# Performance work log

Measured on AMD Instinct MI355X. Metric: run time of the kernel, lower is better.

## Reference

```python
import jax, jax.numpy as jnp
import numpy as np

B, L, H, P = 128, 40, 256, 256   # n_mols, max_num_atoms, pc_hidden, pred_hidden
NS, NC, NB = 40, 5, 5            # n_SYMBOLS, n_FORMAL_CHARGES, n_BOND_TYPES


def _lin(key, fan_in, fan_out):
    kw, kb = jax.random.split(key)
    s = 1.0 / np.sqrt(fan_in)
    W = jax.random.uniform(kw, (fan_out, fan_in), minval=-s, maxval=s, dtype=jnp.float32)
    b = jax.random.uniform(kb, (fan_out,), minval=-s, maxval=s, dtype=jnp.float32)
    return W, b


def setup_inputs() -> dict:
    key = jax.random.key(0)
    ks = jax.random.split(key, 7)
    x = jax.random.normal(ks[0], (B, L, H), dtype=jnp.float32)
    W1s, b1s = _lin(ks[1], H, P)
    W2s, b2s = _lin(ks[2], P, NS)
    W1c, b1c = _lin(ks[3], H, P)
    W2c, b2c = _lin(ks[4], P, NC)
    W1b, b1b = _lin(ks[5], 2 * H, 2 * P)
    W2b, b2b = _lin(ks[6], 2 * P, NB)
    return dict(x_embedding=x, W1s=W1s, b1s=b1s, W2s=W2s, b2s=b2s,
                W1c=W1c, b1c=b1c, W2c=W2c, b2c=b2c,
                W1b=W1b, b1b=b1b, W2b=W2b, b2b=b2b)


def reference(x_embedding, W1s, b1s, W2s, b2s, W1c, b1c, W2c, b2c, W1b, b1b, W2b, b2b):
    lrelu = lambda v: jax.nn.leaky_relu(v, 0.01)
    y = x_embedding  # [B, L, H]; every molecule has ley == L (max_num_atoms)

    # symbol / charge heads: small FFNs applied per atom
    symbols = lrelu(jnp.einsum('blh,ph->blp', y, W1s) + b1s) @ W2s.T + b2s
    symbols = symbols.reshape(-1, NS)                       # [B*L, NS]
    charges = lrelu(jnp.einsum('blh,ph->blp', y, W1c) + b1c) @ W2c.T + b2c
    charges = charges.reshape(-1, NC)                       # [B*L, NC]

    # pairwise bond features: concat(atom_i, atom_j) -> [B, L, L, 2H]
    x1 = jnp.broadcast_to(y[:, :, None, :], (B, L, L, H))
    x2 = jnp.broadcast_to(y[:, None, :, :], (B, L, L, H))
    pair = jnp.concatenate([x1, x2], axis=-1)
    hb = lrelu(jnp.einsum('bijc,pc->bijp', pair, W1b) + b1b)  # [B, L, L, 2P]
    bl = jnp.einsum('bijp,np->bijn', hb, W2b) + b2b           # [B, L, L, NB]
    bl = bl + jnp.swapaxes(bl, 1, 2)                          # symmetrize

    # diagonal override: bond types 0..3 -> -1000, type 4 ('no bond') -> +1000
    eye = jnp.eye(L, dtype=bool)[None, :, :, None]
    diagvals = jnp.array([-1000.0, -1000.0, -1000.0, -1000.0, 1000.0], dtype=bl.dtype)
    bl = jnp.where(eye, diagvals, bl)
    bonds = bl.reshape(-1, NB)                                # [B*L*L, NB]

    return (symbols, charges, bonds)
```

## Files before the change

kernel.cpp:

```cpp
#include <hip/hip_runtime.h>
#include <hip/hip_fp16.h>

#define NMOL 128
#define LMAX 40
#define HDIM 256
#define NSYM 40
#define NCHG 5
#define NROWS (NMOL * LMAX)

typedef __attribute__((ext_vector_type(8))) unsigned short ushx8;
typedef __attribute__((ext_vector_type(8))) _Float16 f16x8;
typedef __attribute__((ext_vector_type(2))) _Float16 f16x2;
typedef __attribute__((ext_vector_type(2))) __fp16 fp16x2r;
typedef __attribute__((ext_vector_type(4))) float f32x4;

__device__ __forceinline__ float lrelu(float x) { return fmaxf(x, 0.01f * x); }

__global__ __launch_bounds__(256) void gemm_kernel(
    const float* __restrict__ x,
    const float* __restrict__ W1s, const float* __restrict__ b1s,
    const float* __restrict__ W1c, const float* __restrict__ b1c,
    const float* __restrict__ W1b, const float* __restrict__ b1b,
    _Float16* __restrict__ hout, _Float16* __restrict__ uvp)
{
    __shared__ _Float16 As[64 * 256];
    __shared__ _Float16 Bs[64 * 256];

    const int t  = threadIdx.x;
    const int m0 = blockIdx.x * 64;
    const int n0 = blockIdx.y * 64;

    const float* Bsrc; int bstride; const float* bias_src;
    if (n0 < 256)       { Bsrc = W1s + (size_t)n0 * 256;            bstride = 256; bias_src = b1s + n0; }
    else if (n0 < 512)  { Bsrc = W1c + (size_t)(n0 - 256) * 256;    bstride = 256; bias_src = b1c + (n0 - 256); }
    else if (n0 < 1024) { Bsrc = W1b + (size_t)(n0 - 512) * 512;    bstride = 512; bias_src = b1b + (n0 - 512); }
    else                { Bsrc = W1b + (size_t)(n0 - 1024) * 512 + 256; bstride = 512; bias_src = nullptr; }

    #pragma unroll
    for (int pass = 0; pass < 8; ++pass) {
        int gch = pass * 256 + t;
        int r = gch >> 5, c = gch & 31;
        int cs = c ^ (r & 7);
        {
            const float* s = x + (size_t)(m0 + r) * 256 + c * 8;
            float4 a0 = *(const float4*)s, a1 = *(const float4*)(s + 4);
            union { f16x8 v; fp16x2r p[4]; } u;
            u.p[0] = __builtin_amdgcn_cvt_pkrtz(a0.x, a0.y);
            u.p[1] = __builtin_amdgcn_cvt_pkrtz(a0.z, a0.w);
            u.p[2] = __builtin_amdgcn_cvt_pkrtz(a1.x, a1.y);
            u.p[3] = __builtin_amdgcn_cvt_pkrtz(a1.z, a1.w);
            *(f16x8*)&As[r * 256 + cs * 8] = u.v;
        }
        {
            const float* s = Bsrc + (size_t)r * bstride + c * 8;
            float4 a0 = *(const float4*)s, a1 = *(const float4*)(s + 4);
            union { f16x8 v; fp16x2r p[4]; } u;
            u.p[0] = __builtin_amdgcn_cvt_pkrtz(a0.x, a0.y);
            u.p[1] = __builtin_amdgcn_cvt_pkrtz(a0.z, a0.w);
            u.p[2] = __builtin_amdgcn_cvt_pkrtz(a1.x, a1.y);
            u.p[3] = __builtin_amdgcn_cvt_pkrtz(a1.z, a1.w);
            *(f16x8*)&Bs[r * 256 + cs * 8] = u.v;
        }
    }
    __syncthreads();

    const int lane = t & 63, wave = t >> 6;
    const int wm = (wave >> 1) * 32, wn = (wave & 1) * 32;
    const int lr = lane & 15, lk = lane >> 4;

    f32x4 acc[2][2] = {};
    #pragma unroll
    for (int ks = 0; ks < 8; ++ks) {
        f16x8 a[2], b[2];
        #pragma unroll
        for (int i = 0; i < 2; ++i) {
            int ra = wm + i * 16 + lr;
            int ca = (ks * 4 + lk) ^ (ra & 7);
            a[i] = *(const f16x8*)&As[ra * 256 + ca * 8];
            int rb = wn + i * 16 + lr;
            int cb = (ks * 4 + lk) ^ (rb & 7);
            b[i] = *(const f16x8*)&Bs[rb * 256 + cb * 8];
        }
        #pragma unroll
        for (int mi = 0; mi < 2; ++mi)
            #pragma unroll
            for (int ni = 0; ni < 2; ++ni)
                acc[mi][ni] = __builtin_amdgcn_mfma_f32_16x16x32_f16(a[mi], b[ni], acc[mi][ni], 0, 0, 0);
    }

    #pragma unroll
    for (int mi = 0; mi < 2; ++mi) {
        #pragma unroll
        for (int ni = 0; ni < 2; ++ni) {
            int nl = wn + ni * 16 + lr;
            int ng = n0 + nl;
            float bs = bias_src ? bias_src[nl] : 0.0f;
            #pragma unroll
            for (int rg = 0; rg < 4; ++rg) {
                int row = m0 + wm + mi * 16 + lk * 4 + rg;
                float v = acc[mi][ni][rg] + bs;
                if (ng < 512) hout[(size_t)row * 512 + ng] = (_Float16)lrelu(v);
                else          uvp[(size_t)row * 1024 + (ng - 512)] = (_Float16)v;
            }
        }
    }
}

__global__ __launch_bounds__(256) void heads2_kernel(
    const _Float16* __restrict__ h,
    const float* __restrict__ W2s, const float* __restrict__ b2s,
    const float* __restrict__ W2c, const float* __restrict__ b2c,
    float* __restrict__ out_sym, float* __restrict__ out_chg)
{
    __shared__ unsigned short hsd[8 * 512];
    const int t = threadIdx.x;
    const int r0 = blockIdx.x * 8;
    #pragma unroll
    for (int pass = 0; pass < 2; ++pass) {
        int ch = pass * 256 + t;
        *(ushx8*)&hsd[ch * 8] = *(const ushx8*)((const unsigned short*)h + (size_t)r0 * 512 + ch * 8);
    }
    __syncthreads();

    for (int idx = t; idx < 8 * (NSYM + NCHG); idx += 256) {
        int r = idx / (NSYM + NCHG), m = idx % (NSYM + NCHG);
        bool is_sym = (m < NSYM);
        int n = is_sym ? m : m - NSYM;
        const unsigned short* hrow = &hsd[r * 512 + (is_sym ? 0 : 256)];
        const float* wrow = is_sym ? (W2s + (size_t)n * 256) : (W2c + (size_t)n * 256);
        float acc = is_sym ? b2s[n] : b2c[n];
        for (int k8 = 0; k8 < 32; ++k8) {
            union { ushx8 u; f16x2 h2[4]; } hh;
            hh.u = *(const ushx8*)&hrow[k8 * 8];
            float4 w0 = *(const float4*)&wrow[k8 * 8];
            float4 w1 = *(const float4*)&wrow[k8 * 8 + 4];
            acc += (float)hh.h2[0][0]*w0.x + (float)hh.h2[0][1]*w0.y
                 + (float)hh.h2[1][0]*w0.z + (float)hh.h2[1][1]*w0.w
                 + (float)hh.h2[2][0]*w1.x + (float)hh.h2[2][1]*w1.y
                 + (float)hh.h2[3][0]*w1.z + (float)hh.h2[3][1]*w1.w;
        }
        int row = r0 + r;
        if (is_sym) out_sym[(size_t)row * NSYM + n] = acc;
        else        out_chg[(size_t)row * NCHG + n] = acc;
    }
}

__global__ __launch_bounds__(512) void bonds_kernel2(
    const _Float16* __restrict__ uv, const float* __restrict__ W2b,
    const float* __restrict__ b2b, float* __restrict__ out_bond)
{
    __shared__ unsigned short kv[40 * 1032];

    const int t   = threadIdx.x;
    const int mol = blockIdx.x >> 1;
    const int hf  = blockIdx.x & 1;
    const unsigned short* uvm = (const unsigned short*)uv + (size_t)mol * 40 * 1024;

    #pragma unroll
    for (int pass = 0; pass < 10; ++pass) {
        int ch = pass * 512 + t;
        int r = ch >> 7, c = ch & 127;
        int cs = c ^ ((r >> 1) & 7);
        *(ushx8*)&kv[r * 1032 + cs * 8] = *(const ushx8*)(uvm + (size_t)r * 1024 + c * 8);
    }
    __syncthreads();

    if (t < 390) {
        int q = hf * 390 + t;
        int i = 0, rem = q;
        while (rem >= 39 - i) { rem -= 39 - i; ++i; }
        int j = i + 1 + rem;

        const int si = (i >> 1) & 7, sj = (j >> 1) & 7;
        const unsigned short* rowi = &kv[i * 1032];
        const unsigned short* rowj = &kv[j * 1032];
        const _Float16 c001 = (_Float16)0.01f;

        float a0 = 0.f, a1 = 0.f, a2 = 0.f, a3 = 0.f, a4 = 0.f;
        for (int p8 = 0; p8 < 64; ++p8) {
            union U8 { ushx8 u; f16x2 h[4]; };
            U8 ui, vi, uj, vj;
            ui.u = *(const ushx8*)&rowi[(p8 ^ si) * 8];
            vi.u = *(const ushx8*)&rowi[(64 + (p8 ^ si)) * 8];
            uj.u = *(const ushx8*)&rowj[(p8 ^ sj) * 8];
            vj.u = *(const ushx8*)&rowj[(64 + (p8 ^ sj)) * 8];
            const float* wp = W2b + p8 * 8;
            #pragma unroll
            for (int k = 0; k < 4; ++k) {
                f16x2 s1 = ui.h[k] + vj.h[k];
                f16x2 s2 = uj.h[k] + vi.h[k];
                f16x2 l1 = __builtin_elementwise_max(s1, s1 * c001);
                f16x2 l2 = __builtin_elementwise_max(s2, s2 * c001);
                f16x2 e  = l1 + l2;
                float ex = (float)e[0], ey = (float)e[1];
                a0 += ex * wp[2*k]        + ey * wp[2*k + 1];
                a1 += ex * wp[512 + 2*k]  + ey * wp[512 + 2*k + 1];
                a2 += ex * wp[1024 + 2*k] + ey * wp[1024 + 2*k + 1];
                a3 += ex * wp[1536 + 2*k] + ey * wp[1536 + 2*k + 1];
                a4 += ex * wp[2048 + 2*k] + ey * wp[2048 + 2*k + 1];
            }
        }
        const int base = mol * LMAX;
        float* o1 = out_bond + ((size_t)(base + i) * LMAX + j) * 5;
        float* o2 = out_bond + ((size_t)(base + j) * LMAX + i) * 5;
        float v0 = a0 + 2.f * b2b[0], v1 = a1 + 2.f * b2b[1], v2 = a2 + 2.f * b2b[2];
        float v3 = a3 + 2.f * b2b[3], v4 = a4 + 2.f * b2b[4];
        o1[0] = v0; o1[1] = v1; o1[2] = v2; o1[3] = v3; o1[4] = v4;
        o2[0] = v0; o2[1] = v1; o2[2] = v2; o2[3] = v3; o2[4] = v4;
    } else if (hf == 0 && t < 390 + LMAX) {
        int d = t - 390;
        float* o = out_bond + ((size_t)(mol * LMAX + d) * LMAX + d) * 5;
        o[0] = -1000.f; o[1] = -1000.f; o[2] = -1000.f; o[3] = -1000.f; o[4] = 1000.f;
    }
}

extern "C" void kernel_launch(void* const* d_in, const int* in_sizes, int n_in,
                              void* d_out, int out_size, void* d_ws, size_t ws_size,
                              hipStream_t stream)
{
    const float* x   = (const float*)d_in[0];
    const float* W1s = (const float*)d_in[1];
    const float* b1s = (const float*)d_in[2];
    const float* W2s = (const float*)d_in[3];
    const float* b2s = (const float*)d_in[4];
    const float* W1c = (const float*)d_in[5];
    const float* b1c = (const float*)d_in[6];
    const float* W2c = (const float*)d_in[7];
    const float* b2c = (const float*)d_in[8];
    const float* W1b = (const float*)d_in[9];
    const float* b1b = (const float*)d_in[10];
    const float* W2b = (const float*)d_in[11];
    const float* b2b = (const float*)d_in[12];

    float* out      = (float*)d_out;
    float* out_sym  = out;
    float* out_chg  = out + (size_t)NROWS * NSYM;
    float* out_bond = out + (size_t)NROWS * (NSYM + NCHG);

    char* ws = (char*)d_ws;
    const size_t H_B = (size_t)NROWS * 512 * 2;
    _Float16* hbuf = (_Float16*)ws;
    _Float16* uvp  = (_Float16*)(ws + H_B);

    dim3 gg(NROWS / 64, 1536 / 64);
    gemm_kernel<<<gg, 256, 0, stream>>>(x, W1s, b1s, W1c, b1c, W1b, b1b, hbuf, uvp);
    bonds_kernel2<<<NMOL * 2, 512, 0, stream>>>(uvp, W2b, b2b, out_bond);
    heads2_kernel<<<NROWS / 8, 256, 0, stream>>>(hbuf, W2s, b2s, W2c, b2c, out_sym, out_chg);
}
```

Before: 162.7 us.

## Fuse head second-layer into bonds kernel; read GEMM weights directly from global

The symbol/charge second-layer work moves into idle waves (threads 448-511) of the bonds kernel, so the separate heads kernel and its launch go away. In the first-layer GEMM the weight tile is no longer staged in shared memory. Each lane loads its fp32 weight fragment from global memory and converts it to fp16 in registers, which halves LDS use and may raise occupancy. In exchange, weight loads become uncoalesced, are repeated per k-step, and sit on the MFMA critical path. The head work is also serialized onto 64 threads per block.

```diff
diff --git a/kernel.cpp b/kernel.cpp
--- a/kernel.cpp
+++ b/kernel.cpp
@@ -24,7 +24,6 @@
     _Float16* __restrict__ hout, _Float16* __restrict__ uvp)
 {
     __shared__ _Float16 As[64 * 256];
-    __shared__ _Float16 Bs[64 * 256];
 
     const int t  = threadIdx.x;
     const int m0 = blockIdx.x * 64;
@@ -41,26 +40,14 @@
         int gch = pass * 256 + t;
         int r = gch >> 5, c = gch & 31;
         int cs = c ^ (r & 7);
-        {
-            const float* s = x + (size_t)(m0 + r) * 256 + c * 8;
-            float4 a0 = *(const float4*)s, a1 = *(const float4*)(s + 4);
-            union { f16x8 v; fp16x2r p[4]; } u;
-            u.p[0] = __builtin_amdgcn_cvt_pkrtz(a0.x, a0.y);
-            u.p[1] = __builtin_amdgcn_cvt_pkrtz(a0.z, a0.w);
-            u.p[2] = __builtin_amdgcn_cvt_pkrtz(a1.x, a1.y);
-            u.p[3] = __builtin_amdgcn_cvt_pkrtz(a1.z, a1.w);
-            *(f16x8*)&As[r * 256 + cs * 8] = u.v;
-        }
-        {
-            const float* s = Bsrc + (size_t)r * bstride + c * 8;
-            float4 a0 = *(const float4*)s, a1 = *(const float4*)(s + 4);
-            union { f16x8 v; fp16x2r p[4]; } u;
-            u.p[0] = __builtin_amdgcn_cvt_pkrtz(a0.x, a0.y);
-            u.p[1] = __builtin_amdgcn_cvt_pkrtz(a0.z, a0.w);
-            u.p[2] = __builtin_amdgcn_cvt_pkrtz(a1.x, a1.y);
-            u.p[3] = __builtin_amdgcn_cvt_pkrtz(a1.z, a1.w);
-            *(f16x8*)&Bs[r * 256 + cs * 8] = u.v;
-        }
+        const float* s = x + (size_t)(m0 + r) * 256 + c * 8;
+        float4 a0 = *(const float4*)s, a1 = *(const float4*)(s + 4);
+        union { f16x8 v; fp16x2r p[4]; } u;
+        u.p[0] = __builtin_amdgcn_cvt_pkrtz(a0.x, a0.y);
+        u.p[1] = __builtin_amdgcn_cvt_pkrtz(a0.z, a0.w);
+        u.p[2] = __builtin_amdgcn_cvt_pkrtz(a1.x, a1.y);
+        u.p[3] = __builtin_amdgcn_cvt_pkrtz(a1.z, a1.w);
+        *(f16x8*)&As[r * 256 + cs * 8] = u.v;
     }
     __syncthreads();
 
@@ -78,8 +65,14 @@
             int ca = (ks * 4 + lk) ^ (ra & 7);
             a[i] = *(const f16x8*)&As[ra * 256 + ca * 8];
             int rb = wn + i * 16 + lr;
-            int cb = (ks * 4 + lk) ^ (rb & 7);
-            b[i] = *(const f16x8*)&Bs[rb * 256 + cb * 8];
+            const float* wr = Bsrc + (size_t)rb * bstride + (ks * 4 + lk) * 8;
+            float4 w0 = *(const float4*)wr, w1 = *(const float4*)(wr + 4);
+            union { f16x8 v; fp16x2r p[4]; } ub;
+            ub.p[0] = __builtin_amdgcn_cvt_pkrtz(w0.x, w0.y);
+            ub.p[1] = __builtin_amdgcn_cvt_pkrtz(w0.z, w0.w);
+            ub.p[2] = __builtin_amdgcn_cvt_pkrtz(w1.x, w1.y);
+            ub.p[3] = __builtin_amdgcn_cvt_pkrtz(w1.z, w1.w);
+            b[i] = ub.v;
         }
         #pragma unroll
         for (int mi = 0; mi < 2; ++mi)
@@ -106,48 +99,13 @@
     }
 }
 
-__global__ __launch_bounds__(256) void heads2_kernel(
-    const _Float16* __restrict__ h,
+__global__ __launch_bounds__(512) void consumer_kernel(
+    const _Float16* __restrict__ uv, const _Float16* __restrict__ h,
+    const float* __restrict__ W2b, const float* __restrict__ b2b,
     const float* __restrict__ W2s, const float* __restrict__ b2s,
     const float* __restrict__ W2c, const float* __restrict__ b2c,
-    float* __restrict__ out_sym, float* __restrict__ out_chg)
-{
-    __shared__ unsigned short hsd[8 * 512];
-    const int t = threadIdx.x;
-    const int r0 = blockIdx.x * 8;
-    #pragma unroll
-    for (int pass = 0; pass < 2; ++pass) {
-        int ch = pass * 256 + t;
-        *(ushx8*)&hsd[ch * 8] = *(const ushx8*)((const unsigned short*)h + (size_t)r0 * 512 + ch * 8);
-    }
-    __syncthreads();
-
-    for (int idx = t; idx < 8 * (NSYM + NCHG); idx += 256) {
-        int r = idx / (NSYM + NCHG), m = idx % (NSYM + NCHG);
-        bool is_sym = (m < NSYM);
-        int n = is_sym ? m : m - NSYM;
-        const unsigned short* hrow = &hsd[r * 512 + (is_sym ? 0 : 256)];
-        const float* wrow = is_sym ? (W2s + (size_t)n * 256) : (W2c + (size_t)n * 256);
-        float acc = is_sym ? b2s[n] : b2c[n];
-        for (int k8 = 0; k8 < 32; ++k8) {
-            union { ushx8 u; f16x2 h2[4]; } hh;
-            hh.u = *(const ushx8*)&hrow[k8 * 8];
-            float4 w0 = *(const float4*)&wrow[k8 * 8];
-            float4 w1 = *(const float4*)&wrow[k8 * 8 + 4];
-            acc += (float)hh.h2[0][0]*w0.x + (float)hh.h2[0][1]*w0.y
-                 + (float)hh.h2[1][0]*w0.z + (float)hh.h2[1][1]*w0.w
-                 + (float)hh.h2[2][0]*w1.x + (float)hh.h2[2][1]*w1.y
-                 + (float)hh.h2[3][0]*w1.z + (float)hh.h2[3][1]*w1.w;
-        }
-        int row = r0 + r;
-        if (is_sym) out_sym[(size_t)row * NSYM + n] = acc;
-        else        out_chg[(size_t)row * NCHG + n] = acc;
-    }
-}
-
-__global__ __launch_bounds__(512) void bonds_kernel2(
-    const _Float16* __restrict__ uv, const float* __restrict__ W2b,
-    const float* __restrict__ b2b, float* __restrict__ out_bond)
+    float* __restrict__ out_sym, float* __restrict__ out_chg,
+    float* __restrict__ out_bond)
 {
     __shared__ unsigned short kv[40 * 1032];
 
@@ -178,7 +136,7 @@
 
         float a0 = 0.f, a1 = 0.f, a2 = 0.f, a3 = 0.f, a4 = 0.f;
         for (int p8 = 0; p8 < 64; ++p8) {
-            union U8 { ushx8 u; f16x2 h[4]; };
+            union U8 { ushx8 u; f16x2 hh[4]; };
             U8 ui, vi, uj, vj;
             ui.u = *(const ushx8*)&rowi[(p8 ^ si) * 8];
             vi.u = *(const ushx8*)&rowi[(64 + (p8 ^ si)) * 8];
@@ -187,8 +145,8 @@
             const float* wp = W2b + p8 * 8;
             #pragma unroll
             for (int k = 0; k < 4; ++k) {
-                f16x2 s1 = ui.h[k] + vj.h[k];
-                f16x2 s2 = uj.h[k] + vi.h[k];
+                f16x2 s1 = ui.hh[k] + vj.hh[k];
+                f16x2 s2 = uj.hh[k] + vi.hh[k];
                 f16x2 l1 = __builtin_elementwise_max(s1, s1 * c001);
                 f16x2 l2 = __builtin_elementwise_max(s2, s2 * c001);
                 f16x2 e  = l1 + l2;
@@ -207,6 +165,30 @@
         float v3 = a3 + 2.f * b2b[3], v4 = a4 + 2.f * b2b[4];
         o1[0] = v0; o1[1] = v1; o1[2] = v2; o1[3] = v3; o1[4] = v4;
         o2[0] = v0; o2[1] = v1; o2[2] = v2; o2[3] = v3; o2[4] = v4;
+    } else if (t >= 448) {
+        const int base = hf * 900;
+        for (int task = base + (t - 448); task < base + 900; task += 64) {
+            int r = task / 45, m = task % 45;
+            bool is_sym = (m < NSYM);
+            int n = is_sym ? m : m - NSYM;
+            const unsigned short* hrow = (const unsigned short*)h
+                + ((size_t)(mol * LMAX + r)) * 512 + (is_sym ? 0 : 256);
+            const float* wrow = is_sym ? (W2s + (size_t)n * 256) : (W2c + (size_t)n * 256);
+            float acc = is_sym ? b2s[n] : b2c[n];
+            for (int k8 = 0; k8 < 32; ++k8) {
+                union { ushx8 u; f16x2 h2[4]; } hh;
+                hh.u = *(const ushx8*)&hrow[k8 * 8];
+                float4 w0 = *(const float4*)&wrow[k8 * 8];
+                float4 w1 = *(const float4*)&wrow[k8 * 8 + 4];
+                acc += (float)hh.h2[0][0]*w0.x + (float)hh.h2[0][1]*w0.y
+                     + (float)hh.h2[1][0]*w0.z + (float)hh.h2[1][1]*w0.w
+                     + (float)hh.h2[2][0]*w1.x + (float)hh.h2[2][1]*w1.y
+                     + (float)hh.h2[3][0]*w1.z + (float)hh.h2[3][1]*w1.w;
+            }
+            int row = mol * LMAX + r;
+            if (is_sym) out_sym[(size_t)row * NSYM + n] = acc;
+            else        out_chg[(size_t)row * NCHG + n] = acc;
+        }
     } else if (hf == 0 && t < 390 + LMAX) {
         int d = t - 390;
         float* o = out_bond + ((size_t)(mol * LMAX + d) * LMAX + d) * 5;
@@ -244,6 +226,7 @@
 
     dim3 gg(NROWS / 64, 1536 / 64);
     gemm_kernel<<<gg, 256, 0, stream>>>(x, W1s, b1s, W1c, b1c, W1b, b1b, hbuf, uvp);
-    bonds_kernel2<<<NMOL * 2, 512, 0, stream>>>(uvp, W2b, b2b, out_bond);
-    heads2_kernel<<<NROWS / 8, 256, 0, stream>>>(hbuf, W2s, b2s, W2c, b2c, out_sym, out_chg);
+    consumer_kernel<<<NMOL * 2, 512, 0, stream>>>(uvp, hbuf, W2b, b2b,
+                                                  W2s, b2s, W2c, b2c,
+                                                  out_sym, out_chg, out_bond);
 }
```

After: 181.6 us. 1.12x slower.
